# Performance work log

Measured on AMD Instinct MI355X. Metric: run time of the kernel, lower is better.

The kernel has to match this reference:

```python
import jax, jax.numpy as jnp
import numpy as np

BS = 32  # block size
EPS = 1e-5

def _bn(h, g, b):
    # training-mode batchnorm over (N,H,W) of the gathered block batch
    mu = h.mean((0, 2, 3), keepdims=True)
    var = h.var((0, 2, 3), keepdims=True)
    return (h - mu) * jax.lax.rsqrt(var + EPS) * g.reshape(1, -1, 1, 1) + b.reshape(1, -1, 1, 1)

def setup_inputs() -> dict:
    key = jax.random.key(0)
    ks = jax.random.split(key, 12)
    B, Cin, H, W, Cout = 4, 128, 256, 256, 256
    Hb, Wb = H // BS, W // BS
    x = jax.random.normal(ks[0], (B, Cin, H, W), dtype=jnp.float32)
    rng = np.random.default_rng(0)
    flat = np.sort(rng.choice(B * Hb * Wb, size=128, replace=False)).astype(np.int32)
    bi = flat // (Hb * Wb)
    by = (flat % (Hb * Wb)) // Wb
    bx = flat % Wb
    block_idx = jnp.asarray(np.stack([bi, by, bx], axis=1), dtype=jnp.int32)  # [Nact,3]
    s1 = 1.0 / np.sqrt(Cin)
    s2 = 1.0 / np.sqrt(Cout * 9)
    return {
        "x": x,
        "w1": jax.random.normal(ks[1], (Cout, Cin), jnp.float32) * s1,
        "b1": jnp.zeros((Cout,), jnp.float32),
        "g1": jnp.ones((Cout,), jnp.float32),
        "be1": jnp.zeros((Cout,), jnp.float32),
        "w2": jax.random.normal(ks[2], (Cout, Cout, 3, 3), jnp.float32) * s2,
        "b2": jnp.zeros((Cout,), jnp.float32),
        "g2": jnp.ones((Cout,), jnp.float32),
        "be2": jnp.zeros((Cout,), jnp.float32),
        "wd": jax.random.normal(ks[3], (Cout, Cin), jnp.float32) * s1,
        "bd": jnp.zeros((Cout,), jnp.float32),
        "block_idx": block_idx,
    }

def reference(x, w1, b1, g1, be1, w2, b2, g2, be2, wd, bd, block_idx):
    B, Cin, H, W = x.shape
    Cout = w1.shape[0]
    Hb, Wb = H // BS, W // BS
    # --- sparse gather: [Nact, Cin, BS, BS] ---
    xb = x.reshape(B, Cin, Hb, BS, Wb, BS).transpose(0, 2, 4, 1, 3, 5)
    xb = xb.reshape(B * Hb * Wb, Cin, BS, BS)
    flat = block_idx[:, 0] * (Hb * Wb) + block_idx[:, 1] * Wb + block_idx[:, 2]
    dense = xb[flat]
    # --- dense conv stack on active blocks ---
    h = jnp.einsum('nchw,oc->nohw', dense, w1) + b1.reshape(1, -1, 1, 1)
    h = jax.nn.relu(_bn(h, g1, be1))  # relu is inplace in torch -> feeds conv2
    h = jax.lax.conv_general_dilated(h, w2, (1, 1), 'SAME',
                                     dimension_numbers=('NCHW', 'OIHW', 'NCHW'))
    h = h + b2.reshape(1, -1, 1, 1)
    dense_y = jax.nn.relu(_bn(h, g2, be2))
    # NOTE: original conv3/bn3 output is dead code (scatter uses dense_y); omitted.
    # --- dense base path (in_channels != out_channels -> downsample 1x1 conv) ---
    ybase = jnp.einsum('nchw,oc->nohw', x, wd) + bd.reshape(1, -1, 1, 1)
    # --- sparse scatter (overwrite, add=False) ---
    yb = ybase.reshape(B, Cout, Hb, BS, Wb, BS).transpose(0, 2, 4, 1, 3, 5)
    yb = yb.reshape(B * Hb * Wb, Cout, BS, BS)
    yb = yb.at[flat].set(dense_y)
    y = yb.reshape(B, Hb, Wb, Cout, BS, BS).transpose(0, 3, 1, 4, 2, 5)
    return y.reshape(B, Cout, H, W)
```

## Files before the change

### kernel.cpp

```cpp
#include <hip/hip_runtime.h>
#include <stdint.h>

#define CIN  128
#define COUT 256
#define HH   256
#define WW   256
#define BSZ  32
#define HB   8
#define WB   8
#define NBLK 256
#define P2   34
#define PIX2 1156

typedef __attribute__((ext_vector_type(8))) short bfx8;
typedef __attribute__((ext_vector_type(4))) float f32x4;

#define MFMA(a,b,c) __builtin_amdgcn_mfma_f32_16x16x32_bf16((a),(b),(c),0,0,0)

typedef const __attribute__((address_space(1))) unsigned int gu32;
typedef __attribute__((address_space(3))) unsigned int lu32;
#define GLOAD16(g, p) __builtin_amdgcn_global_load_lds((gu32*)(g), (lu32*)(p), 16, 0, 0)

static __device__ __forceinline__ float bf2f(unsigned short u){
  union { unsigned int i; float f; } v; v.i = ((unsigned int)u)<<16; return v.f;
}
static __device__ __forceinline__ unsigned short f2bf(float f){
  union { float f; unsigned int i; } v; v.f = f;
  unsigned int r = v.i + 0x7fffu + ((v.i>>16)&1u);
  return (unsigned short)(r>>16);
}

__global__ void k_prep(const float* __restrict__ w1, const float* __restrict__ wd,
                       const float* __restrict__ w2,
                       unsigned short* __restrict__ w1b, unsigned short* __restrict__ wdb,
                       unsigned short* __restrict__ w2t){
  int i = blockIdx.x*256 + threadIdx.x;
  if (i < COUT*CIN){ w1b[i] = f2bf(w1[i]); wdb[i] = f2bf(wd[i]); }
  if (i < COUT*COUT*9){
    int co = i/2304, r = i - co*2304;
    int ci = r/9,   tp = r - ci*9;
    w2t[((size_t)tp*COUT + co)*COUT + ci] = f2bf(w2[i]);
  }
}

__global__ void k_lists(const int* __restrict__ bidx, int nact,
                        int* __restrict__ flags, int* __restrict__ inact){
  int t = threadIdx.x;
  if (t < nact){
    int f = bidx[t*3]*(HB*WB) + bidx[t*3+1]*WB + bidx[t*3+2];
    flags[f] = 1;
  }
  __syncthreads();
  if (t == 0){
    int c = 0;
    for (int f = 0; f < NBLK; ++f) if (!flags[f]) inact[c++] = f;
  }
}

template<int MODE>
__global__ __launch_bounds__(256) void k_gemm1(
    const float* __restrict__ x, const unsigned short* __restrict__ wgt,
    const int* __restrict__ bidx, const int* __restrict__ inact,
    const float* __restrict__ bd, unsigned short* __restrict__ h1p,
    float* __restrict__ out, float* __restrict__ part){
  __shared__ unsigned short lds[2*5120];
  int rg = blockIdx.x, cot = blockIdx.y, z = blockIdx.z;
  int bi, by, bx;
  if (MODE == 0){ bi = bidx[z*3]; by = bidx[z*3+1]; bx = bidx[z*3+2]; }
  else { int fl = inact[z]; bi = fl>>6; by = (fl>>3)&7; bx = fl&7; }
  int t = threadIdx.x, l = t&63, wid = t>>6;
  int wc = wid>>1, wp = wid&1;
  int y0 = rg*4;
  int co_w = cot*128 + wc*64;

  const unsigned short* wb = wgt + (size_t)(co_w + (l&15))*CIN + ((l>>4)*8);
  bfx8 wfrag[4][4];
  #pragma unroll
  for (int kc = 0; kc < 4; ++kc)
    #pragma unroll
    for (int m = 0; m < 4; ++m)
      wfrag[kc][m] = *(const bfx8*)(wb + kc*32 + (size_t)m*16*CIN);

  const float* xb = x + (size_t)bi*CIN*HH*WW + (size_t)(by*BSZ + y0)*WW + bx*BSZ;
  float4 ra[2], rb_[2];
  auto ldreg = [&](int kc){
    #pragma unroll
    for (int j = 0; j < 2; ++j){
      int u = j*256 + t;
      int ci0 = (u>>5)*2 + kc*32;
      int p = (u&31)*4;
      const float* s = xb + (size_t)ci0*(HH*WW) + (p>>5)*WW + (p&31);
      ra[j]  = *(const float4*)s;
      rb_[j] = *(const float4*)(s + HH*WW);
    }
  };
  auto wrlds = [&](int buf){
    #pragma unroll
    for (int j = 0; j < 2; ++j){
      int u = j*256 + t;
      int ci0 = (u>>5)*2;
      int p = (u&31)*4;
      unsigned short* d = &lds[buf*5120 + ci0];
      *(ushort2*)&d[(p+0)*40] = make_ushort2(f2bf(ra[j].x), f2bf(rb_[j].x));
      *(ushort2*)&d[(p+1)*40] = make_ushort2(f2bf(ra[j].y), f2bf(rb_[j].y));
      *(ushort2*)&d[(p+2)*40] = make_ushort2(f2bf(ra[j].z), f2bf(rb_[j].z));
      *(ushort2*)&d[(p+3)*40] = make_ushort2(f2bf(ra[j].w), f2bf(rb_[j].w));
    }
  };

  f32x4 acc[4][4] = {};
  ldreg(0);
  for (int kc = 0; kc < 4; ++kc){
    wrlds(kc&1);
    if (kc < 3) ldreg(kc+1);
    __syncthreads();
    const unsigned short* lb = &lds[(kc&1)*5120];
    #pragma unroll
    for (int f = 0; f < 4; ++f){
      bfx8 b = *(const bfx8*)&lb[(wp*64 + f*16 + (l&15))*40 + (l>>4)*8];
      acc[0][f] = MFMA(wfrag[kc][0], b, acc[0][f]);
      acc[1][f] = MFMA(wfrag[kc][1], b, acc[1][f]);
      acc[2][f] = MFMA(wfrag[kc][2], b, acc[2][f]);
      acc[3][f] = MFMA(wfrag[kc][3], b, acc[3][f]);
    }
  }

  #pragma unroll
  for (int m = 0; m < 4; ++m){
    int co = co_w + m*16 + ((l>>4)<<2);
    #pragma unroll
    for (int f = 0; f < 4; ++f){
      int px = wp*64 + f*16 + (l&15);
      int ly = px>>5, lx = px&31;
      if (MODE == 0){
        *(ushort4*)&h1p[((size_t)z*PIX2 + (size_t)(y0+ly+1)*P2 + (lx+1))*COUT + co] =
          make_ushort4(f2bf(acc[m][f][0]), f2bf(acc[m][f][1]),
                       f2bf(acc[m][f][2]), f2bf(acc[m][f][3]));
      } else {
        int gy = by*BSZ + y0 + ly, gx = bx*BSZ + lx;
        #pragma unroll
        for (int j = 0; j < 4; ++j)
          out[(((size_t)bi*COUT + co + j)*HH + gy)*WW + gx] = acc[m][f][j] + bd[co+j];
      }
    }
  }

  if (MODE == 0){
    float s_[4][4], q_[4][4];
    #pragma unroll
    for (int m = 0; m < 4; ++m)
      #pragma unroll
      for (int j = 0; j < 4; ++j){
        float s = 0.f, q = 0.f;
        #pragma unroll
        for (int f = 0; f < 4; ++f){ float v = acc[m][f][j]; s += v; q += v*v; }
        s_[m][j] = s; q_[m][j] = q;
      }
    #pragma unroll
    for (int off = 1; off < 16; off <<= 1)
      #pragma unroll
      for (int m = 0; m < 4; ++m)
        #pragma unroll
        for (int j = 0; j < 4; ++j){
          s_[m][j] += __shfl_xor(s_[m][j], off);
          q_[m][j] += __shfl_xor(q_[m][j], off);
        }
    if ((l&15) == 0){
      int grp = z & 15;
      #pragma unroll
      for (int m = 0; m < 4; ++m)
        #pragma unroll
        for (int j = 0; j < 4; ++j){
          int co = co_w + m*16 + ((l>>4)<<2) + j;
          atomicAdd(&part[((size_t)grp*COUT + co)*2],   s_[m][j]);
          atomicAdd(&part[((size_t)grp*COUT + co)*2+1], q_[m][j]);
        }
    }
  }
}

__global__ void k_fin(const float* __restrict__ part, const float* __restrict__ g,
                      const float* __restrict__ be, float* __restrict__ st, float inv){
  int t = threadIdx.x;
  float s = 0.f, q = 0.f;
  #pragma unroll
  for (int gi = 0; gi < 16; ++gi){
    s += part[((size_t)gi*COUT + t)*2];
    q += part[((size_t)gi*COUT + t)*2+1];
  }
  float mu = s*inv, var = q*inv - mu*mu;
  float sc = g[t]*rsqrtf(var + 1e-5f);
  st[t] = sc; st[256+t] = be[t] - mu*sc;
}

__global__ void k_bn1(unsigned short* __restrict__ h1p, const float* __restrict__ st, int total){
  int t = threadIdx.x;
  int ci0 = (t&31)*8;
  float sc[8], tc[8];
  #pragma unroll
  for (int j = 0; j < 8; ++j){ sc[j] = st[ci0+j]; tc[j] = st[256+ci0+j]; }
  #pragma unroll
  for (int it = 0; it < 4; ++it){
    int gpix = blockIdx.x*32 + it*8 + (t>>5);
    if (gpix >= total) continue;
    int n = gpix/PIX2; int p = gpix - n*PIX2;
    int row = p/P2, col = p - row*P2;
    unsigned short* addr = h1p + (size_t)gpix*COUT + ci0;
    if (row >= 1 && row <= 32 && col >= 1 && col <= 32){
      bfx8 v = *(bfx8*)addr;
      unsigned short o[8];
      #pragma unroll
      for (int j = 0; j < 8; ++j){
        float f = bf2f(((unsigned short*)&v)[j]);
        o[j] = f2bf(fmaxf(f*sc[j] + tc[j], 0.f));
      }
      *(bfx8*)addr = *(bfx8*)o;
    } else {
      bfx8 z = {};
      *(bfx8*)addr = z;
    }
  }
}

__global__ __launch_bounds__(512, 2) void k_conv2(
    const unsigned short* __restrict__ h1p, const unsigned short* __restrict__ w2t,
    const int* __restrict__ bidx, float* __restrict__ out, float* __restrict__ part){
  __shared__ unsigned short lds[65536];
  int q = blockIdx.x, n = blockIdx.y;
  int bi = bidx[n*3], by = bidx[n*3+1], bx = bidx[n*3+2];
  int t = threadIdx.x, l = t&63, wid = t>>6;
  int wm = wid>>2, wn = wid&3;
  int y0 = q*8;

  int offA[4], offB[4];
  #pragma unroll
  for (int r4 = 0; r4 < 4; ++r4){
    int i = r4*512 + t;
    int row = i>>3, sl_ = i&7;
    int ss = sl_ ^ (row&7);
    offA[r4] = row*COUT + ss*8;
    offB[r4] = ((row>>5)*P2 + (row&31))*COUT + ss*8;
  }
  const unsigned short* h1b = h1p + ((size_t)n*PIX2 + (size_t)y0*P2)*COUT;

  auto stage = [&](int buf, int ks){
    int tp = ks>>2, cc = ks&3;
    int dy = tp/3, dx = tp - dy*3;
    const unsigned short* wsrc = w2t + (size_t)tp*COUT*COUT + cc*64;
    const unsigned short* psrc = h1b + (size_t)(dy*P2 + dx)*COUT + cc*64;
    #pragma unroll
    for (int r4 = 0; r4 < 4; ++r4){
      GLOAD16(wsrc + offA[r4], &lds[buf*32768 + (r4*512 + t)*8]);
      GLOAD16(psrc + offB[r4], &lds[buf*32768 + 16384 + (r4*512 + t)*8]);
    }
  };

  int lr = l&15, lh = l>>4, lx7 = l&7;
  f32x4 acc[8][4] = {};

  stage(0, 0);
  __syncthreads();
  for (int ks = 0; ks < 36; ++ks){
    int cur = ks&1;
    if (ks < 35) stage(cur^1, ks+1);
    const unsigned short* Ab = &lds[cur*32768];
    const unsigned short* Bb = &lds[cur*32768 + 16384];
    bfx8 bf[4][2];
    #pragma unroll
    for (int nn = 0; nn < 4; ++nn)
      #pragma unroll
      for (int kk = 0; kk < 2; ++kk)
        bf[nn][kk] = *(const bfx8*)&Bb[(wn*64 + nn*16 + lr)*64 + ((kk*4 + lh) ^ lx7)*8];
    #pragma unroll
    for (int m = 0; m < 8; ++m){
      bfx8 a0 = *(const bfx8*)&Ab[(wm*128 + m*16 + lr)*64 + ((    lh) ^ lx7)*8];
      bfx8 a1 = *(const bfx8*)&Ab[(wm*128 + m*16 + lr)*64 + ((4 + lh) ^ lx7)*8];
      #pragma unroll
      for (int nn = 0; nn < 4; ++nn){
        acc[m][nn] = MFMA(a0, bf[nn][0], acc[m][nn]);
        acc[m][nn] = MFMA(a1, bf[nn][1], acc[m][nn]);
      }
    }
    __syncthreads();
  }

  #pragma unroll
  for (int m = 0; m < 8; ++m){
    int co = wm*128 + m*16 + lh*4;
    #pragma unroll
    for (int nn = 0; nn < 4; ++nn){
      int px = wn*64 + nn*16 + lr;
      int gy = by*BSZ + y0 + (px>>5), gx = bx*BSZ + (px&31);
      #pragma unroll
      for (int j = 0; j < 4; ++j)
        out[(((size_t)bi*COUT + co + j)*HH + gy)*WW + gx] = acc[m][nn][j];
    }
  }

  #pragma unroll
  for (int m = 0; m < 8; ++m){
    #pragma unroll
    for (int j = 0; j < 4; ++j){
      float s = 0.f, qq = 0.f;
      #pragma unroll
      for (int nn = 0; nn < 4; ++nn){ float v = acc[m][nn][j]; s += v; qq += v*v; }
      #pragma unroll
      for (int off = 1; off < 16; off <<= 1){
        s  += __shfl_xor(s,  off);
        qq += __shfl_xor(qq, off);
      }
      if (lr == 0){
        int co = wm*128 + m*16 + lh*4 + j;
        atomicAdd(&part[((size_t)(n&15)*COUT + co)*2],   s);
        atomicAdd(&part[((size_t)(n&15)*COUT + co)*2+1], qq);
      }
    }
  }
}

__global__ void k_bn2(float* __restrict__ out, const int* __restrict__ bidx,
                      const float* __restrict__ st){
  int cq = blockIdx.x, n = blockIdx.y, t = threadIdx.x;
  int bi = bidx[n*3], by = bidx[n*3+1], bx = bidx[n*3+2];
  int px0 = t*4; int ly = px0>>5, lx = px0&31;
  float* base = out + (size_t)bi*COUT*HH*WW + (size_t)(by*BSZ+ly)*WW + bx*BSZ + lx;
  for (int c = 0; c < 64; ++c){
    int co = cq*64 + c;
    float sc = st[co], tc = st[256+co];
    float4* p = (float4*)(base + (size_t)co*HH*WW);
    float4 v = *p;
    v.x = fmaxf(v.x*sc+tc, 0.f); v.y = fmaxf(v.y*sc+tc, 0.f);
    v.z = fmaxf(v.z*sc+tc, 0.f); v.w = fmaxf(v.w*sc+tc, 0.f);
    *p = v;
  }
}

extern "C" void kernel_launch(void* const* d_in, const int* in_sizes, int n_in,
                              void* d_out, int out_size, void* d_ws, size_t ws_size,
                              hipStream_t stream){
  const float* x   = (const float*)d_in[0];
  const float* w1  = (const float*)d_in[1];
  const float* g1  = (const float*)d_in[3];
  const float* be1 = (const float*)d_in[4];
  const float* w2  = (const float*)d_in[5];
  const float* g2  = (const float*)d_in[7];
  const float* be2 = (const float*)d_in[8];
  const float* wd  = (const float*)d_in[9];
  const float* bd  = (const float*)d_in[10];
  const int* bidx  = (const int*)d_in[11];
  float* out = (float*)d_out;
  const int nact = in_sizes[11]/3;
  const int ninact = NBLK - nact;

  char* wsp = (char*)d_ws;
  size_t off = 0;
  auto carve = [&](size_t bytes)->char*{
    char* p = wsp + off; off += (bytes + 255) & ~(size_t)255; return p;
  };
  unsigned short* h1p = (unsigned short*)carve((size_t)nact*PIX2*COUT*2 + 4096);
  unsigned short* w1b = (unsigned short*)carve((size_t)COUT*CIN*2);
  unsigned short* wdb = (unsigned short*)carve((size_t)COUT*CIN*2);
  unsigned short* w2t = (unsigned short*)carve((size_t)9*COUT*COUT*2);
  float* s1t1  = (float*)carve(512*4);
  float* s2t2  = (float*)carve(512*4);
  float* part1 = (float*)carve((size_t)16*COUT*2*4);
  float* part2 = (float*)carve((size_t)16*COUT*2*4);
  int* flags   = (int*)carve(NBLK*4);
  int* inact   = (int*)carve(NBLK*4);

  hipMemsetAsync(flags, 0, NBLK*4, stream);
  hipMemsetAsync(part1, 0, (size_t)16*COUT*2*4, stream);
  hipMemsetAsync(part2, 0, (size_t)16*COUT*2*4, stream);
  k_lists<<<1, 256, 0, stream>>>(bidx, nact, flags, inact);
  k_prep<<<2304, 256, 0, stream>>>(w1, wd, w2, w1b, wdb, w2t);
  k_gemm1<0><<<dim3(8, 2, nact), 256, 0, stream>>>(x, w1b, bidx, inact, bd, h1p, out, part1);
  k_fin<<<1, 256, 0, stream>>>(part1, g1, be1, s1t1, 1.0f/((float)nact*1024.0f));
  {
    int total = nact*PIX2;
    k_bn1<<<(total + 31)/32, 256, 0, stream>>>(h1p, s1t1, total);
  }
  k_conv2<<<dim3(4, nact), 512, 0, stream>>>(h1p, w2t, bidx, out, part2);
  k_fin<<<1, 256, 0, stream>>>(part2, g2, be2, s2t2, 1.0f/((float)nact*1024.0f));
  if (ninact > 0)
    k_gemm1<1><<<dim3(8, 2, ninact), 256, 0, stream>>>(x, wdb, bidx, inact, bd, h1p, out, part1);
  k_bn2<<<dim3(4, nact), 256, 0, stream>>>(out, bidx, s2t2);
}
```

Before: 458.2 us.

## Restructure conv2 GEMM mainloop into fine-grained interleaved load/MFMA pipeline

Replaces the simple double-buffered conv2 K loop with a manually unrolled two-stage loop. Global-to-LDS loads for the weight (A) and patch (B) tiles are split into halves and issued between MFMA sub-phases, with explicit vmcnt/lgkmcnt waits, s_barrier, sched_barrier and setprio around MFMA bursts. The B tile is prefetched two steps ahead, so copies overlap compute more finely and fewer waits stall the wave. The cost is more barriers per step and fragile hand-written wait counts that could race if they are wrong.

```diff
diff --git a/kernel.cpp b/kernel.cpp
--- a/kernel.cpp
+++ b/kernel.cpp
@@ -243,45 +243,112 @@
   }
   const unsigned short* h1b = h1p + ((size_t)n*PIX2 + (size_t)y0*P2)*COUT;
 
-  auto stage = [&](int buf, int ks){
+  auto stageA = [&](int buf, int ks, int h){
+    int tp = ks>>2, cc = ks&3;
+    const unsigned short* wsrc = w2t + (size_t)tp*COUT*COUT + cc*64;
+    #pragma unroll
+    for (int r4 = 2*h; r4 < 2*h+2; ++r4)
+      GLOAD16(wsrc + offA[r4], &lds[buf*32768 + (r4*512 + t)*8]);
+  };
+  auto stageB = [&](int buf, int ks, int h){
     int tp = ks>>2, cc = ks&3;
     int dy = tp/3, dx = tp - dy*3;
-    const unsigned short* wsrc = w2t + (size_t)tp*COUT*COUT + cc*64;
     const unsigned short* psrc = h1b + (size_t)(dy*P2 + dx)*COUT + cc*64;
     #pragma unroll
-    for (int r4 = 0; r4 < 4; ++r4){
-      GLOAD16(wsrc + offA[r4], &lds[buf*32768 + (r4*512 + t)*8]);
+    for (int r4 = 2*h; r4 < 2*h+2; ++r4)
       GLOAD16(psrc + offB[r4], &lds[buf*32768 + 16384 + (r4*512 + t)*8]);
-    }
   };
 
   int lr = l&15, lh = l>>4, lx7 = l&7;
   f32x4 acc[8][4] = {};
-
-  stage(0, 0);
-  __syncthreads();
-  for (int ks = 0; ks < 36; ++ks){
-    int cur = ks&1;
-    if (ks < 35) stage(cur^1, ks+1);
-    const unsigned short* Ab = &lds[cur*32768];
-    const unsigned short* Bb = &lds[cur*32768 + 16384];
-    bfx8 bf[4][2];
-    #pragma unroll
-    for (int nn = 0; nn < 4; ++nn)
-      #pragma unroll
-      for (int kk = 0; kk < 2; ++kk)
-        bf[nn][kk] = *(const bfx8*)&Bb[(wn*64 + nn*16 + lr)*64 + ((kk*4 + lh) ^ lx7)*8];
-    #pragma unroll
-    for (int m = 0; m < 8; ++m){
-      bfx8 a0 = *(const bfx8*)&Ab[(wm*128 + m*16 + lr)*64 + ((    lh) ^ lx7)*8];
-      bfx8 a1 = *(const bfx8*)&Ab[(wm*128 + m*16 + lr)*64 + ((4 + lh) ^ lx7)*8];
-      #pragma unroll
-      for (int nn = 0; nn < 4; ++nn){
-        acc[m][nn] = MFMA(a0, bf[nn][0], acc[m][nn]);
-        acc[m][nn] = MFMA(a1, bf[nn][1], acc[m][nn]);
-      }
-    }
-    __syncthreads();
+  bfx8 bf[4][2];
+
+  stageB(0, 0, 0); stageB(0, 0, 1);
+  stageA(0, 0, 0); stageA(0, 0, 1);
+  stageB(1, 1, 0); stageB(1, 1, 1);
+  asm volatile("s_waitcnt vmcnt(0)" ::: "memory");
+  __builtin_amdgcn_s_barrier();
+
+  for (int it = 0; it < 18; ++it){
+    int s1 = 2*it+1, s2 = 2*it+2, s3 = 2*it+3;
+    {
+      const unsigned short* Ab = &lds[0];
+      const unsigned short* Bb = &lds[16384];
+      #pragma unroll
+      for (int mp = 0; mp < 4; ++mp){
+        if (mp == 0){
+          #pragma unroll
+          for (int nn = 0; nn < 4; ++nn)
+            #pragma unroll
+            for (int kk = 0; kk < 2; ++kk)
+              bf[nn][kk] = *(const bfx8*)&Bb[(wn*64 + nn*16 + lr)*64 + ((kk*4 + lh) ^ lx7)*8];
+        }
+        int m0 = 2*mp;
+        bfx8 a00 = *(const bfx8*)&Ab[(wm*128 + m0*16 + lr)*64 + ((    lh) ^ lx7)*8];
+        bfx8 a01 = *(const bfx8*)&Ab[(wm*128 + m0*16 + lr)*64 + ((4 + lh) ^ lx7)*8];
+        bfx8 a10 = *(const bfx8*)&Ab[(wm*128 + (m0+1)*16 + lr)*64 + ((    lh) ^ lx7)*8];
+        bfx8 a11 = *(const bfx8*)&Ab[(wm*128 + (m0+1)*16 + lr)*64 + ((4 + lh) ^ lx7)*8];
+        if (mp == 0){ stageA(1, s1, 0); }
+        if (mp == 1){ stageA(1, s1, 1); if (s2 < 36) stageB(0, s2, 0); }
+        if (mp == 2){ if (s2 < 36) stageB(0, s2, 1); }
+        if (mp == 3){
+          if (it < 17) asm volatile("s_waitcnt vmcnt(4)" ::: "memory");
+          else         asm volatile("s_waitcnt vmcnt(0)" ::: "memory");
+        }
+        __builtin_amdgcn_s_barrier();
+        asm volatile("s_waitcnt lgkmcnt(0)" ::: "memory");
+        __builtin_amdgcn_sched_barrier(0);
+        __builtin_amdgcn_s_setprio(1);
+        #pragma unroll
+        for (int nn = 0; nn < 4; ++nn){
+          acc[m0][nn]   = MFMA(a00, bf[nn][0], acc[m0][nn]);
+          acc[m0][nn]   = MFMA(a01, bf[nn][1], acc[m0][nn]);
+          acc[m0+1][nn] = MFMA(a10, bf[nn][0], acc[m0+1][nn]);
+          acc[m0+1][nn] = MFMA(a11, bf[nn][1], acc[m0+1][nn]);
+        }
+        __builtin_amdgcn_s_setprio(0);
+        __builtin_amdgcn_s_barrier();
+      }
+    }
+    {
+      const unsigned short* Ab = &lds[32768];
+      const unsigned short* Bb = &lds[32768 + 16384];
+      #pragma unroll
+      for (int mp = 0; mp < 4; ++mp){
+        if (mp == 0){
+          #pragma unroll
+          for (int nn = 0; nn < 4; ++nn)
+            #pragma unroll
+            for (int kk = 0; kk < 2; ++kk)
+              bf[nn][kk] = *(const bfx8*)&Bb[(wn*64 + nn*16 + lr)*64 + ((kk*4 + lh) ^ lx7)*8];
+        }
+        int m0 = 2*mp;
+        bfx8 a00 = *(const bfx8*)&Ab[(wm*128 + m0*16 + lr)*64 + ((    lh) ^ lx7)*8];
+        bfx8 a01 = *(const bfx8*)&Ab[(wm*128 + m0*16 + lr)*64 + ((4 + lh) ^ lx7)*8];
+        bfx8 a10 = *(const bfx8*)&Ab[(wm*128 + (m0+1)*16 + lr)*64 + ((    lh) ^ lx7)*8];
+        bfx8 a11 = *(const bfx8*)&Ab[(wm*128 + (m0+1)*16 + lr)*64 + ((4 + lh) ^ lx7)*8];
+        if (mp == 0){ if (s2 < 36) stageA(0, s2, 0); }
+        if (mp == 1){ if (s2 < 36) stageA(0, s2, 1); }
+        if (mp == 2){ if (s3 < 36) stageB(1, s3, 0); }
+        if (mp == 3){
+          if (s3 < 36) stageB(1, s3, 1);
+          asm volatile("s_waitcnt vmcnt(4)" ::: "memory");
+        }
+        __builtin_amdgcn_s_barrier();
+        asm volatile("s_waitcnt lgkmcnt(0)" ::: "memory");
+        __builtin_amdgcn_sched_barrier(0);
+        __builtin_amdgcn_s_setprio(1);
+        #pragma unroll
+        for (int nn = 0; nn < 4; ++nn){
+          acc[m0][nn]   = MFMA(a00, bf[nn][0], acc[m0][nn]);
+          acc[m0][nn]   = MFMA(a01, bf[nn][1], acc[m0][nn]);
+          acc[m0+1][nn] = MFMA(a10, bf[nn][0], acc[m0+1][nn]);
+          acc[m0+1][nn] = MFMA(a11, bf[nn][1], acc[m0+1][nn]);
+        }
+        __builtin_amdgcn_s_setprio(0);
+        __builtin_amdgcn_s_barrier();
+      }
+    }
   }
 
   #pragma unroll
```

Result: no change. 458.4 us (+0.0%).

## Halve conv2 pixel tile, single-buffer LDS, and raise occupancy to 4 blocks/CU

Applied to the files above, without the earlier changes.

Each conv2 workgroup now computes 256 channels x 128 pixels instead of 256 x 256, with twice as many workgroups launched. Per-wave accumulators drop from 8x4 to 4x4 tiles and the double-buffered LDS staging becomes one buffer bracketed by two barriers. Launch bounds go from 2 to 4 blocks per CU. The goal is more parallel workgroups and higher occupancy to hide latency, at the cost of losing the explicit load/compute overlap and reloading the weight tile twice as often.

```diff
diff --git a/kernel.cpp b/kernel.cpp
--- a/kernel.cpp
+++ b/kernel.cpp
@@ -222,74 +222,71 @@
   }
 }
 
-__global__ __launch_bounds__(512, 2) void k_conv2(
+__global__ __launch_bounds__(512, 4) void k_conv2(
     const unsigned short* __restrict__ h1p, const unsigned short* __restrict__ w2t,
     const int* __restrict__ bidx, float* __restrict__ out, float* __restrict__ part){
-  __shared__ unsigned short lds[65536];
-  int q = blockIdx.x, n = blockIdx.y;
+  __shared__ unsigned short lds[24576];
+  int bxid = blockIdx.x, n = blockIdx.y;
+  int h = bxid & 1, q = bxid >> 1;
   int bi = bidx[n*3], by = bidx[n*3+1], bx = bidx[n*3+2];
   int t = threadIdx.x, l = t&63, wid = t>>6;
-  int wm = wid>>2, wn = wid&3;
+  int wm = wid>>1, wn = wid&1;
   int y0 = q*8;
 
-  int offA[4], offB[4];
-  #pragma unroll
-  for (int r4 = 0; r4 < 4; ++r4){
-    int i = r4*512 + t;
+  int offA[4], offB[2];
+  #pragma unroll
+  for (int j = 0; j < 4; ++j){
+    int i = j*512 + t;
     int row = i>>3, sl_ = i&7;
-    int ss = sl_ ^ (row&7);
-    offA[r4] = row*COUT + ss*8;
-    offB[r4] = ((row>>5)*P2 + (row&31))*COUT + ss*8;
-  }
-  const unsigned short* h1b = h1p + ((size_t)n*PIX2 + (size_t)y0*P2)*COUT;
-
-  auto stage = [&](int buf, int ks){
-    int tp = ks>>2, cc = ks&3;
+    offA[j] = row*COUT + (sl_ ^ (row&7))*8;
+  }
+  #pragma unroll
+  for (int j = 0; j < 2; ++j){
+    int i = j*512 + t;
+    int row = i>>3, sl_ = i&7;
+    offB[j] = ((row>>5)*P2 + (row&31))*COUT + (sl_ ^ (row&7))*8;
+  }
+  const unsigned short* h1q = h1p + ((size_t)n*PIX2 + (size_t)(y0 + h*4)*P2)*COUT;
+
+  int lr = l&15, lh = l>>4;
+  f32x4 acc[4][4] = {};
+
+  for (int s = 0; s < 36; ++s){
+    int tp = s>>2, cc = s&3;
     int dy = tp/3, dx = tp - dy*3;
     const unsigned short* wsrc = w2t + (size_t)tp*COUT*COUT + cc*64;
-    const unsigned short* psrc = h1b + (size_t)(dy*P2 + dx)*COUT + cc*64;
-    #pragma unroll
-    for (int r4 = 0; r4 < 4; ++r4){
-      GLOAD16(wsrc + offA[r4], &lds[buf*32768 + (r4*512 + t)*8]);
-      GLOAD16(psrc + offB[r4], &lds[buf*32768 + 16384 + (r4*512 + t)*8]);
-    }
-  };
-
-  int lr = l&15, lh = l>>4, lx7 = l&7;
-  f32x4 acc[8][4] = {};
-
-  stage(0, 0);
-  __syncthreads();
-  for (int ks = 0; ks < 36; ++ks){
-    int cur = ks&1;
-    if (ks < 35) stage(cur^1, ks+1);
-    const unsigned short* Ab = &lds[cur*32768];
-    const unsigned short* Bb = &lds[cur*32768 + 16384];
-    bfx8 bf[4][2];
-    #pragma unroll
-    for (int nn = 0; nn < 4; ++nn)
-      #pragma unroll
-      for (int kk = 0; kk < 2; ++kk)
-        bf[nn][kk] = *(const bfx8*)&Bb[(wn*64 + nn*16 + lr)*64 + ((kk*4 + lh) ^ lx7)*8];
-    #pragma unroll
-    for (int m = 0; m < 8; ++m){
-      bfx8 a0 = *(const bfx8*)&Ab[(wm*128 + m*16 + lr)*64 + ((    lh) ^ lx7)*8];
-      bfx8 a1 = *(const bfx8*)&Ab[(wm*128 + m*16 + lr)*64 + ((4 + lh) ^ lx7)*8];
-      #pragma unroll
-      for (int nn = 0; nn < 4; ++nn){
-        acc[m][nn] = MFMA(a0, bf[nn][0], acc[m][nn]);
-        acc[m][nn] = MFMA(a1, bf[nn][1], acc[m][nn]);
-      }
-    }
+    const unsigned short* psrc = h1q + (size_t)(dy*P2 + dx)*COUT + cc*64;
     __syncthreads();
-  }
-
-  #pragma unroll
-  for (int m = 0; m < 8; ++m){
-    int co = wm*128 + m*16 + lh*4;
+    #pragma unroll
+    for (int j = 0; j < 4; ++j)
+      GLOAD16(wsrc + offA[j], &lds[(j*512 + t)*8]);
+    #pragma unroll
+    for (int j = 0; j < 2; ++j)
+      GLOAD16(psrc + offB[j], &lds[16384 + (j*512 + t)*8]);
+    __syncthreads();
+    #pragma unroll
+    for (int kk = 0; kk < 2; ++kk){
+      bfx8 af[4], bfr[4];
+      #pragma unroll
+      for (int m = 0; m < 4; ++m)
+        af[m] = *(const bfx8*)&lds[(wm*64 + m*16 + lr)*64 + ((kk*4 + lh) ^ (lr&7))*8];
+      #pragma unroll
+      for (int nn = 0; nn < 4; ++nn)
+        bfr[nn] = *(const bfx8*)&lds[16384 + (wn*64 + nn*16 + lr)*64 + ((kk*4 + lh) ^ (lr&7))*8];
+      #pragma unroll
+      for (int m = 0; m < 4; ++m)
+        #pragma unroll
+        for (int nn = 0; nn < 4; ++nn)
+          acc[m][nn] = MFMA(af[m], bfr[nn], acc[m][nn]);
+    }
+  }
+
+  #pragma unroll
+  for (int m = 0; m < 4; ++m){
+    int co = wm*64 + m*16 + lh*4;
     #pragma unroll
     for (int nn = 0; nn < 4; ++nn){
-      int px = wn*64 + nn*16 + lr;
+      int px = h*128 + wn*64 + nn*16 + lr;
       int gy = by*BSZ + y0 + (px>>5), gx = bx*BSZ + (px&31);
       #pragma unroll
       for (int j = 0; j < 4; ++j)
@@ -298,7 +295,7 @@
   }
 
   #pragma unroll
-  for (int m = 0; m < 8; ++m){
+  for (int m = 0; m < 4; ++m){
     #pragma unroll
     for (int j = 0; j < 4; ++j){
       float s = 0.f, qq = 0.f;
@@ -310,7 +307,7 @@
         qq += __shfl_xor(qq, off);
       }
       if (lr == 0){
-        int co = wm*128 + m*16 + lh*4 + j;
+        int co = wm*64 + m*16 + lh*4 + j;
         atomicAdd(&part[((size_t)(n&15)*COUT + co)*2],   s);
         atomicAdd(&part[((size_t)(n&15)*COUT + co)*2+1], qq);
       }
@@ -379,7 +376,7 @@
     int total = nact*PIX2;
     k_bn1<<<(total + 31)/32, 256, 0, stream>>>(h1p, s1t1, total);
   }
-  k_conv2<<<dim3(4, nact), 512, 0, stream>>>(h1p, w2t, bidx, out, part2);
+  k_conv2<<<dim3(8, nact), 512, 0, stream>>>(h1p, w2t, bidx, out, part2);
   k_fin<<<1, 256, 0, stream>>>(part2, g2, be2, s2t2, 1.0f/((float)nact*1024.0f));
   if (ninact > 0)
     k_gemm1<1><<<dim3(8, 2, ninact), 256, 0, stream>>>(x, wdb, bidx, inact, bd, h1p, out, part1);
```

Measured after the change: 431.5 us. 5.8% less time.
